# Optimization experiments

Measured on AMD Instinct MI355X. Metric: run time of the kernel, lower is better.

The kernel has to match this reference:

```python
import jax
import jax.numpy as jnp
import numpy as np
from jax import lax

B, NS, T, H, V = 4, 96, 8, 256, 32000
L = NS * T
N = NS + 1                    # num_nodes = num_statements + 1 (exit node)
NUM_LAYERS = NS // 16         # avg_statements_per_step = 16 -> 6 execution steps


def _lstm(c, h, x, Wx, Wh, b):
    """flax-style LSTM cell: gates in (i, f, g, o) order."""
    z = x @ Wx + h @ Wh + b
    gi, gf, gg, go = jnp.split(z, 4, axis=-1)
    c2 = jax.nn.sigmoid(gf) * c + jax.nn.sigmoid(gi) * jnp.tanh(gg)
    h2 = jax.nn.sigmoid(go) * jnp.tanh(c2)
    return c2, h2


def _forward(code_statements, code_length, embed, Wx_s, Wh_s, b_s, W_se, b_se,
             Wx_e, Wh_e, b_e, W_hk, b_hk, W_sd, b_sd, W_d1, b_d1, init_a, init_b):
    # ---- statement embedding: LSTM over the T tokens of each statement ----
    tok = embed[code_statements.astype(jnp.int32)]            # [B, L, H]
    tok = jnp.transpose(tok.reshape(B * NS, T, H), (1, 0, 2))  # [T, B*NS, H]
    c0 = jnp.zeros((B * NS, H), tok.dtype)

    def scan_fn(carry, x):
        c, hh = carry
        c, hh = _lstm(c, hh, x, Wx_s, Wh_s, b_s)
        return (c, hh), None

    (_, h_last), _ = lax.scan(scan_fn, (c0, c0), tok)
    stmt = h_last.reshape(B, NS, H)                           # [B, NS, H]

    # ---- skip encoder: pairwise segment-sum embedding for skipping i -> j ----
    node = jnp.concatenate([stmt, jnp.zeros((B, 1, H), stmt.dtype)], axis=1)  # [B,N,H]
    pref = jnp.concatenate(
        [jnp.zeros((B, 1, H), stmt.dtype), jnp.cumsum(node, axis=1)], axis=1)[:, :N]
    skip = (pref[:, None, :, :] - pref[:, :, None, :]) @ W_se + b_se  # [B,N,N,H]

    stmt_len = (code_length // T).astype(jnp.int32)           # exit node index per example

    # ---- execution loop with soft instruction pointer ----
    c = jnp.broadcast_to(init_a, (B, N, H))
    h = jnp.broadcast_to(init_b, (B, N, H))
    p = jnp.zeros((B, N)).at[:, 0].set(1.0)

    def step(c, h, p, skip_nnh, length, layer):
        # per-example: c,h [N,H]; p [N]; skip_nnh [N,N,H]; length scalar
        n = p.shape[0]
        ar = jnp.arange(n)
        if layer == 0:
            mask = jnp.zeros((n, n)).at[:, 1].set(1.0)
        elif layer == NUM_LAYERS - 1:
            mask = jnp.zeros((n, n)).at[:, length].set(1.0)   # force skip to exit
        else:
            mask = 1.0 - jnp.tri(n)                           # strictly forward skips
            mask = jnp.where(ar <= length, mask, 0.0)         # no skips past exit
            mask = mask.at[:, length].set(1.0)                # always allow exit

        # skip attention logits
        skip_keys = skip_nnh @ W_sd + b_sd                    # [N,N,H]
        h_key = h @ W_hk + b_hk                               # [N,H]
        act = jax.nn.relu(jnp.concatenate(
            [jnp.broadcast_to(h_key[:, None, :], (n, n, H)), skip_keys], axis=-1))
        skip_logits = jnp.squeeze(act @ W_d1, -1) + b_d1[0]   # [N,N]
        skip_logits = jnp.where(mask > 0, skip_logits, -jnp.inf)
        skip_p = jax.nn.softmax(skip_logits, axis=-1)

        # one LSTM skip-execution step for every (i, j) pair, vectorized
        z = skip_nnh @ Wx_e + (h @ Wh_e)[:, None, :] + b_e    # [N,N,4H]
        gi, gf, gg, go = jnp.split(z, 4, axis=-1)
        c_prop = jax.nn.sigmoid(gf) * c[:, None, :] + jax.nn.sigmoid(gi) * jnp.tanh(gg)
        h_prop = jax.nn.sigmoid(go) * jnp.tanh(c_prop)
        fwd_edge = (ar[None, :] > ar[:, None])[:, :, None]    # only j > i executes
        c_prop = jnp.where(fwd_edge, c_prop, c[:, None, :])
        h_prop = jnp.where(fwd_edge, h_prop, h[:, None, :])
        valid = (mask[:, :, None] > 0) & (p[:, None, None] > 0)
        c_prop = jnp.where(valid, c_prop, 0.0)
        h_prop = jnp.where(valid, h_prop, 0.0)

        # soft aggregation of proposals weighted by p(i) * skip_p(i -> j)
        w = skip_p * p[:, None]                               # [N,N]
        denom = (w.sum(axis=0) + 1e-7)[:, None]               # [N,1]
        c_new = jnp.einsum('ijh,ij->jh', c_prop, w) / denom
        h_new = jnp.einsum('ijh,ij->jh', h_prop, w) / denom
        p_new = p @ skip_p
        return c_new, h_new, p_new

    for layer in range(NUM_LAYERS):
        c, h, p = jax.vmap(step, in_axes=(0, 0, 0, 0, 0, None))(
            c, h, p, skip, stmt_len, layer)
    return h                                                  # [B, N, H]


def setup_inputs() -> dict:
    key = jax.random.key(0)
    ks = jax.random.split(key, 16)

    def dense(k, fi, fo):
        return jax.random.normal(k, (fi, fo)) * (1.0 / np.sqrt(fi))

    return {
        'code_statements': jax.random.randint(ks[0], (B, L), 0, V, dtype=jnp.int32),
        'code_length': jax.random.randint(ks[1], (B,), 64, L, dtype=jnp.int32),
        'embed': jax.random.normal(ks[2], (V, H)) * 0.02,
        'Wx_s': dense(ks[3], H, 4 * H), 'Wh_s': dense(ks[4], H, 4 * H),
        'b_s': jnp.zeros((4 * H,)),
        'W_se': dense(ks[5], H, H), 'b_se': jnp.zeros((H,)),
        'Wx_e': dense(ks[6], H, 4 * H), 'Wh_e': dense(ks[7], H, 4 * H),
        'b_e': jnp.zeros((4 * H,)),
        'W_hk': dense(ks[8], H, H), 'b_hk': jnp.zeros((H,)),
        'W_sd': dense(ks[9], H, H), 'b_sd': jnp.zeros((H,)),
        'W_d1': dense(ks[10], 2 * H, 1), 'b_d1': jnp.zeros((1,)),
        'init_a': jax.random.normal(ks[11], (H,)),
        'init_b': jax.random.normal(ks[12], (H,)),
    }


def reference(code_statements, code_length, embed, Wx_s, Wh_s, b_s, W_se, b_se,
              Wx_e, Wh_e, b_e, W_hk, b_hk, W_sd, b_sd, W_d1, b_d1, init_a, init_b):
    return _forward(code_statements, code_length, embed, Wx_s, Wh_s, b_s, W_se, b_se,
                    Wx_e, Wh_e, b_e, W_hk, b_hk, W_sd, b_sd, W_d1, b_d1, init_a, init_b)
```

## Files before the change

### kernel.cpp

```cpp
#include <hip/hip_runtime.h>
#include <cstddef>

#define B_   4
#define NS_  96
#define T_   8
#define H_   256
#define N_   97
#define NL_  6
#define R_   388

__device__ __forceinline__ float sigm(float x) {
    return __builtin_amdgcn_rcpf(1.0f + __builtin_amdgcn_exp2f(-1.44269504f * x));
}
__device__ __forceinline__ float tanh_f(float x) {
    return 1.0f - 2.0f * __builtin_amdgcn_rcpf(1.0f + __builtin_amdgcn_exp2f(2.88539008f * x));
}

__device__ __forceinline__ void fma16(float4 a, float4 w0, float4 w1, float4 w2,
                                      float4 w3, float* acc) {
    acc[0] = fmaf(a.x, w0.x, acc[0]); acc[1] = fmaf(a.x, w0.y, acc[1]);
    acc[2] = fmaf(a.x, w0.z, acc[2]); acc[3] = fmaf(a.x, w0.w, acc[3]);
    acc[0] = fmaf(a.y, w1.x, acc[0]); acc[1] = fmaf(a.y, w1.y, acc[1]);
    acc[2] = fmaf(a.y, w1.z, acc[2]); acc[3] = fmaf(a.y, w1.w, acc[3]);
    acc[0] = fmaf(a.z, w2.x, acc[0]); acc[1] = fmaf(a.z, w2.y, acc[1]);
    acc[2] = fmaf(a.z, w2.z, acc[2]); acc[3] = fmaf(a.z, w2.w, acc[3]);
    acc[0] = fmaf(a.w, w3.x, acc[0]); acc[1] = fmaf(a.w, w3.y, acc[1]);
    acc[2] = fmaf(a.w, w3.z, acc[2]); acc[3] = fmaf(a.w, w3.w, acc[3]);
}

__global__ __launch_bounds__(512) void prologue(
        const int* __restrict__ ids, const float* __restrict__ embed,
        const float* __restrict__ Wx_s, const float* __restrict__ b_s,
        const float* __restrict__ b_se, const float* __restrict__ Wx_e,
        const float* __restrict__ b_e, const float* __restrict__ W_sd,
        const float* __restrict__ b_sd, const float* __restrict__ Wh_e,
        const float* __restrict__ init_a, const float* __restrict__ init_b,
        float* __restrict__ xz, float* __restrict__ cz, float* __restrict__ ck,
        float* __restrict__ hw, float* __restrict__ c0, float* __restrict__ h0,
        float* __restrict__ p0) {
    int bid = blockIdx.x, t = threadIdx.x;
    if (bid < 384) {
        __shared__ float As[64][260];
        __shared__ int ridx[64];
        int r0 = (bid >> 3) * 64, n0 = (bid & 7) * 128;
        if (t < 64) ridx[t] = ids[r0 + t];
        __syncthreads();
#pragma unroll
        for (int m = 0; m < 8; m++) {
            int L = m * 512 + t;
            int r = L >> 6, c4 = (L & 63) * 4;
            *(float4*)&As[r][c4] = *(const float4*)(embed + (size_t)ridx[r] * 256 + c4);
        }
        __syncthreads();
        int rg = t >> 5, cg = t & 31;
        float acc[4][4] = {};
        const float* wp = Wx_s + n0 + 4 * cg;
#pragma unroll 4
        for (int kb = 0; kb < 64; kb++) {
            float4 w0 = *(const float4*)(wp + (size_t)(4 * kb + 0) * 1024);
            float4 w1 = *(const float4*)(wp + (size_t)(4 * kb + 1) * 1024);
            float4 w2 = *(const float4*)(wp + (size_t)(4 * kb + 2) * 1024);
            float4 w3 = *(const float4*)(wp + (size_t)(4 * kb + 3) * 1024);
#pragma unroll
            for (int i = 0; i < 4; i++) {
                float4 a = *(const float4*)&As[rg * 4 + i][4 * kb];
                fma16(a, w0, w1, w2, w3, acc[i]);
            }
        }
        int col = n0 + 4 * cg;
        float4 bv = *(const float4*)&b_s[col];
#pragma unroll
        for (int i = 0; i < 4; i++) {
            int r = r0 + rg * 4 + i;
            float4 o = make_float4(acc[i][0] + bv.x, acc[i][1] + bv.y,
                                   acc[i][2] + bv.z, acc[i][3] + bv.w);
            *(float4*)&xz[(size_t)r * 1024 + col] = o;
        }
    } else if (bid < 386) {
        int n = (bid - 384) * 512 + t;
        float acc = b_e[n];
        for (int k = 0; k < 256; k++) acc = fmaf(b_se[k], Wx_e[(size_t)k * 1024 + n], acc);
        cz[n] = acc;
    } else if (bid < 388) {
        int n = (bid - 386) * 512 + t;
        float acc = b_e[n];
        for (int k = 0; k < 256; k++) {
            acc = fmaf(b_se[k], Wx_e[(size_t)k * 1024 + n], acc);
            acc = fmaf(init_b[k], Wh_e[(size_t)k * 1024 + n], acc);
        }
        hw[n] = acc;
    } else if (bid == 388) {
        if (t < 256) {
            float acc = b_sd[t];
            for (int k = 0; k < 256; k++) acc = fmaf(b_se[k], W_sd[(size_t)k * 256 + t], acc);
            ck[t] = acc;
        }
    } else {
        int r0 = (bid - 389) * 8 + (t >> 8) * 4;
        int col = t & 255;
        float ia = init_a[col], ib = init_b[col];
#pragma unroll
        for (int rr = 0; rr < 4; rr++) {
            int row = r0 + rr;
            if (row < R_) {
                c0[(size_t)row * 256 + col] = ia;
                h0[(size_t)row * 256 + col] = ib;
                if (col == 0) p0[row] = ((row % N_) == 0) ? 1.0f : 0.0f;
            }
        }
    }
}

__global__ __launch_bounds__(256) void lstm_first(const float* __restrict__ xz,
        const float* __restrict__ Wh, float* __restrict__ hbuf, float* __restrict__ cbuf) {
    __shared__ float Wh_s[256][64];
    __shared__ float h_s[32][260];
    __shared__ float zs[32][68];
    int t = threadIdx.x;
    int ct = blockIdx.x, st = blockIdx.y;
    int et0 = ct * 16, s0 = st * 32;
#pragma unroll
    for (int m = 0; m < 16; m++) {
        int L = m * 256 + t;
        int k = L >> 4, f = L & 15;
        int gg = f >> 2, qq = f & 3;
        *(float4*)&Wh_s[k][f * 4] = *(const float4*)&Wh[(size_t)k * 1024 + gg * 256 + et0 + qq * 4];
    }
    for (int seq = 0; seq < 32; seq++) {
        const float* z0 = xz + ((size_t)(s0 + seq) * T_) * 1024;
        float gi = z0[t], gg = z0[512 + t], go = z0[768 + t];
        float c0v = sigm(gi) * tanh_f(gg);
        h_s[seq][t] = sigm(go) * tanh_f(c0v);
    }
    float creg[2];
    {
        int sqA = t >> 4, e = et0 + (t & 15);
#pragma unroll
        for (int u = 0; u < 2; u++) {
            const float* z0 = xz + ((size_t)(s0 + sqA + u * 16) * T_) * 1024;
            creg[u] = sigm(z0[e]) * tanh_f(z0[512 + e]);
        }
    }
    __syncthreads();
    {
        int sp = (t >> 4) & 15, cq = t & 15;
        int g = cq >> 2, q4 = cq & 3;
        int gcol = g * 256 + et0 + q4 * 4;
        float4 a0 = *(const float4*)(xz + ((size_t)(s0 + sp) * T_ + 1) * 1024 + gcol);
        float4 a1 = *(const float4*)(xz + ((size_t)(s0 + sp + 16) * T_ + 1) * 1024 + gcol);
#pragma unroll 4
        for (int k = 0; k < 256; k++) {
            float4 w4 = *(const float4*)&Wh_s[k][cq * 4];
            float hA = h_s[sp][k];
            float hB = h_s[sp + 16][k];
            a0.x = fmaf(hA, w4.x, a0.x); a0.y = fmaf(hA, w4.y, a0.y);
            a0.z = fmaf(hA, w4.z, a0.z); a0.w = fmaf(hA, w4.w, a0.w);
            a1.x = fmaf(hB, w4.x, a1.x); a1.y = fmaf(hB, w4.y, a1.y);
            a1.z = fmaf(hB, w4.z, a1.z); a1.w = fmaf(hB, w4.w, a1.w);
        }
        *(float4*)&zs[sp][cq * 4] = a0;
        *(float4*)&zs[sp + 16][cq * 4] = a1;
    }
    __syncthreads();
    {
        int sqA = t >> 4, e = t & 15;
#pragma unroll
        for (int u = 0; u < 2; u++) {
            int seq = sqA + u * 16;
            float gi = zs[seq][e], gf = zs[seq][16 + e], gg = zs[seq][32 + e], go = zs[seq][48 + e];
            float cn = sigm(gf) * creg[u] + sigm(gi) * tanh_f(gg);
            size_t gidx = (size_t)(s0 + seq) * H_ + et0 + e;
            cbuf[gidx] = cn;
            hbuf[gidx] = sigm(go) * tanh_f(cn);
        }
    }
}

__global__ __launch_bounds__(256) void lstm_step(int step, const float* __restrict__ xz,
        const float* __restrict__ Wh, float* __restrict__ hbuf, float* __restrict__ cbuf) {
    __shared__ float Wh_s[256][64];
    __shared__ float h_s[32][260];
    __shared__ float zs[32][68];
    int t = threadIdx.x;
    int ct = blockIdx.x, st = blockIdx.y;
    int et0 = ct * 16, s0 = st * 32;
    int sp = t >> 4, cq = t & 15;
    int g = cq >> 2, q4 = cq & 3;
    int gcol = g * 256 + et0 + q4 * 4;
    float4 a0 = *(const float4*)(xz + ((size_t)(s0 + sp) * T_ + step) * 1024 + gcol);
    float4 a1 = *(const float4*)(xz + ((size_t)(s0 + sp + 16) * T_ + step) * 1024 + gcol);
#pragma unroll
    for (int m = 0; m < 16; m++) {
        int L = m * 256 + t;
        int k = L >> 4, f = L & 15;
        int gg = f >> 2, qq = f & 3;
        *(float4*)&Wh_s[k][f * 4] = *(const float4*)&Wh[(size_t)k * 1024 + gg * 256 + et0 + qq * 4];
    }
#pragma unroll
    for (int m = 0; m < 8; m++) {
        int L = m * 256 + t;
        int seq = L >> 6, c4 = (L & 63) * 4;
        *(float4*)&h_s[seq][c4] = *(const float4*)&hbuf[(size_t)(s0 + seq) * H_ + c4];
    }
    __syncthreads();
#pragma unroll 4
    for (int k = 0; k < 256; k++) {
        float4 w4 = *(const float4*)&Wh_s[k][cq * 4];
        float h0 = h_s[sp][k];
        float h1 = h_s[sp + 16][k];
        a0.x = fmaf(h0, w4.x, a0.x); a0.y = fmaf(h0, w4.y, a0.y);
        a0.z = fmaf(h0, w4.z, a0.z); a0.w = fmaf(h0, w4.w, a0.w);
        a1.x = fmaf(h1, w4.x, a1.x); a1.y = fmaf(h1, w4.y, a1.y);
        a1.z = fmaf(h1, w4.z, a1.z); a1.w = fmaf(h1, w4.w, a1.w);
    }
    *(float4*)&zs[sp][cq * 4] = a0;
    *(float4*)&zs[sp + 16][cq * 4] = a1;
    __syncthreads();
    int seqA = t >> 4, e = t & 15;
#pragma unroll
    for (int u = 0; u < 2; u++) {
        int seq = seqA + u * 16;
        float gi = zs[seq][e], gf = zs[seq][16 + e], gg = zs[seq][32 + e], go = zs[seq][48 + e];
        size_t gidx = (size_t)(s0 + seq) * H_ + et0 + e;
        float cnew = sigm(gf) * cbuf[gidx] + sigm(gi) * tanh_f(gg);
        cbuf[gidx] = cnew;
        hbuf[gidx] = sigm(go) * tanh_f(cnew);
    }
}

template<int MT>
__global__ __launch_bounds__(256) void gemm_t(const float* __restrict__ A,
        const float* __restrict__ W, const float* __restrict__ bias,
        const float* __restrict__ subQ, const float* __restrict__ pgate,
        float* __restrict__ C, int R, int NC) {
    __shared__ float As[MT][260];
    __shared__ int anyflag;
    int t = threadIdx.x;
    int n0 = blockIdx.x * 128;
    int r0 = blockIdx.y * MT;
    if (pgate) {
        if (t == 0) anyflag = 0;
        __syncthreads();
        if (t < MT && r0 + t < R && pgate[r0 + t] != 0.0f) anyflag = 1;
        __syncthreads();
        if (!anyflag) return;
    }
#pragma unroll
    for (int m = 0; m < MT / 4; m++) {
        int L = m * 256 + t;
        int r = L >> 6, c4 = (L & 63) * 4;
        int rr = r0 + r;
        float4 v = make_float4(0.f, 0.f, 0.f, 0.f);
        if (rr < R) v = *(const float4*)(A + (size_t)rr * 256 + c4);
        *(float4*)&As[r][c4] = v;
    }
    __syncthreads();
    constexpr int RT = MT / 8;
    int rg = t >> 5, cg = t & 31;
    float acc[RT][4] = {};
    const float* wp = W + n0 + 4 * cg;
#pragma unroll 2
    for (int kb = 0; kb < 64; kb++) {
        float4 w0 = *(const float4*)(wp + (size_t)(4 * kb + 0) * NC);
        float4 w1 = *(const float4*)(wp + (size_t)(4 * kb + 1) * NC);
        float4 w2 = *(const float4*)(wp + (size_t)(4 * kb + 2) * NC);
        float4 w3 = *(const float4*)(wp + (size_t)(4 * kb + 3) * NC);
#pragma unroll
        for (int i = 0; i < RT; i++) {
            float4 a = *(const float4*)&As[rg * RT + i][4 * kb];
            fma16(a, w0, w1, w2, w3, acc[i]);
        }
    }
    int col = n0 + 4 * cg;
    float4 bv = make_float4(0.f, 0.f, 0.f, 0.f);
    if (bias) bv = *(const float4*)&bias[col];
#pragma unroll
    for (int i = 0; i < RT; i++) {
        int r = r0 + rg * RT + i;
        if (r < R) {
            float4 o = make_float4(acc[i][0] + bv.x, acc[i][1] + bv.y,
                                   acc[i][2] + bv.z, acc[i][3] + bv.w);
            if (subQ) {
                float4 s4 = *(const float4*)(subQ + (size_t)r * NC + col);
                o.x -= s4.x; o.y -= s4.y; o.z -= s4.z; o.w -= s4.w;
            }
            *(float4*)&C[(size_t)r * NC + col] = o;
        }
    }
}

__global__ __launch_bounds__(256) void qr_kernel(const float* __restrict__ S,
        const float* __restrict__ Wx_e, const float* __restrict__ W_sd,
        const float* __restrict__ hw, float* __restrict__ q, float* __restrict__ ve0,
        float* __restrict__ r_, float* __restrict__ rT) {
    __shared__ float As[16][260];
    int t = threadIdx.x;
    int bx = blockIdx.x;
    int r0 = blockIdx.y * 16;
#pragma unroll
    for (int m = 0; m < 4; m++) {
        int L = m * 256 + t;
        int r = L >> 6, c4 = (L & 63) * 4;
        int rr = r0 + r;
        float4 v = make_float4(0.f, 0.f, 0.f, 0.f);
        if (rr < R_) v = *(const float4*)(S + (size_t)rr * 256 + c4);
        *(float4*)&As[r][c4] = v;
    }
    __syncthreads();
    bool isq = bx < 8;
    const float* W = isq ? Wx_e : W_sd;
    int NC = isq ? 1024 : 256;
    int n0 = (isq ? bx : bx - 8) * 128;
    int rg = t >> 5, cg = t & 31;
    float acc[2][4] = {};
    const float* wp = W + n0 + 4 * cg;
#pragma unroll 2
    for (int kb = 0; kb < 64; kb++) {
        float4 w0 = *(const float4*)(wp + (size_t)(4 * kb + 0) * NC);
        float4 w1 = *(const float4*)(wp + (size_t)(4 * kb + 1) * NC);
        float4 w2 = *(const float4*)(wp + (size_t)(4 * kb + 2) * NC);
        float4 w3 = *(const float4*)(wp + (size_t)(4 * kb + 3) * NC);
#pragma unroll
        for (int i = 0; i < 2; i++) {
            float4 a = *(const float4*)&As[rg * 2 + i][4 * kb];
            fma16(a, w0, w1, w2, w3, acc[i]);
        }
    }
    int col = n0 + 4 * cg;
#pragma unroll
    for (int i = 0; i < 2; i++) {
        int r = r0 + rg * 2 + i;
        if (r < R_) {
            float4 o = make_float4(acc[i][0], acc[i][1], acc[i][2], acc[i][3]);
            if (isq) {
                *(float4*)&q[(size_t)r * 1024 + col] = o;
                float4 hwv = *(const float4*)&hw[col];
                float4 v0 = make_float4(hwv.x - o.x, hwv.y - o.y, hwv.z - o.z, hwv.w - o.w);
                *(float4*)&ve0[(size_t)r * 1024 + col] = v0;
            } else {
                *(float4*)&r_[(size_t)r * 256 + col] = o;
                int b = r / N_, n = r - b * N_;
                rT[((size_t)b * 256 + col + 0) * 128 + n] = o.x;
                rT[((size_t)b * 256 + col + 1) * 128 + n] = o.y;
                rT[((size_t)b * 256 + col + 2) * 128 + n] = o.z;
                rT[((size_t)b * 256 + col + 3) * 128 + n] = o.w;
            }
        }
    }
}

__global__ __launch_bounds__(1024) void cumsum_k(const float* __restrict__ stmt,
                                                 float* __restrict__ pref) {
    __shared__ float buf[96][256];
    int b = blockIdx.x, t = threadIdx.x;
#pragma unroll
    for (int m = 0; m < 6; m++) {
        int L = m * 1024 + t;
        int r = L >> 6, c4 = (L & 63) * 4;
        *(float4*)&buf[r][c4] = *(const float4*)(stmt + ((size_t)b * NS_ + r) * 256 + c4);
    }
    __syncthreads();
    if (t < 256) {
        float run = 0.0f;
        pref[((size_t)b * N_) * H_ + t] = 0.0f;
        for (int n = 1; n < N_; n++) {
            run += buf[n - 1][t];
            pref[((size_t)b * N_ + n) * H_ + t] = run;
        }
    }
}

__global__ void softmax_once(const float* __restrict__ r, const float* __restrict__ rT,
                             const float* __restrict__ ck, const float* __restrict__ Wd1,
                             const int* __restrict__ code_length,
                             float* __restrict__ spT_mid, float* __restrict__ spT0,
                             float* __restrict__ spT5) {
    __shared__ float ri[H_], ckl[H_], wd[H_];
    __shared__ float part[8][128];
    __shared__ float red[4];
    int t = threadIdx.x;
    int j = t & 127, half = t >> 7;
    int bi = blockIdx.x;
    int b = bi / N_, i = bi % N_;
    if (t < H_) {
        ri[t] = r[(size_t)bi * H_ + t];
        ckl[t] = ck[t];
        wd[t] = Wd1[256 + t];
    }
    __syncthreads();
    int len = code_length[b] / T_;
    bool valid = (j < N_) && ((j > i && j <= len) || (j == len));
    float acc = 0.0f;
    if (valid) {
        const float* rTb = rT + (size_t)b * H_ * 128 + j;
        int h0 = half * 32;
#pragma unroll 4
        for (int hh = 0; hh < 32; hh++) {
            int h = h0 + hh;
            float v = rTb[(size_t)h * 128] - ri[h] + ckl[h];
            acc = fmaf(fmaxf(v, 0.0f), wd[h], acc);
        }
    }
    part[half][j] = acc;
    __syncthreads();
    float logit = -3.0e38f;
    if (t < 128) {
        if (valid)
            logit = part[0][j] + part[1][j] + part[2][j] + part[3][j]
                  + part[4][j] + part[5][j] + part[6][j] + part[7][j];
        float m = logit;
#pragma unroll
        for (int off = 32; off; off >>= 1) m = fmaxf(m, __shfl_xor(m, off));
        if ((t & 63) == 0) red[t >> 6] = m;
    }
    __syncthreads();
    float e = 0.0f;
    if (t < 128) {
        float m = fmaxf(red[0], red[1]);
        e = valid ? __builtin_amdgcn_exp2f(1.44269504f * (logit - m)) : 0.0f;
        float s = e;
#pragma unroll
        for (int off = 32; off; off >>= 1) s += __shfl_xor(s, off);
        if ((t & 63) == 0) red[2 + (t >> 6)] = s;
    }
    __syncthreads();
    if (t < 128 && j < N_) {
        float s = red[2] + red[3];
        size_t o = ((size_t)b * N_ + j) * 128 + i;
        spT_mid[o] = e / s;
        spT0[o] = (j == 1) ? 1.0f : 0.0f;
        spT5[o] = (j == len) ? 1.0f : 0.0f;
    }
}

__global__ __launch_bounds__(512) void aggregate(const float* __restrict__ q,
        const float* __restrict__ ve, const float* __restrict__ spT,
        const float* __restrict__ p, const float* __restrict__ cc,
        const float* __restrict__ hc, float* __restrict__ cn,
        float* __restrict__ hn, float* __restrict__ pn) {
    __shared__ float qj[1024];
    __shared__ float wcol[128];
    __shared__ int vlist[128];
    __shared__ int cnts[2];
    __shared__ float wsums[2];
    __shared__ float parts[2][2][H_];
    int t = threadIdx.x;
    int bj = blockIdx.x;
    int b = bj / N_, j = bj - b * N_;
    bool pred = false;
    int rank = 0;
    if (t < 128) {
        float wv = (t < N_) ? spT[(size_t)bj * 128 + t] * p[b * N_ + t] : 0.f;
        wcol[t] = wv;
        float s = wv;
#pragma unroll
        for (int off = 32; off; off >>= 1) s += __shfl_xor(s, off);
        pred = (wv != 0.0f);
        unsigned long long mask = __ballot(pred);
        int lane = t & 63;
        rank = __popcll(mask & ((1ull << lane) - 1ull));
        if (lane == 0) { cnts[t >> 6] = (int)__popcll(mask); wsums[t >> 6] = s; }
    }
    __syncthreads();
    float wsum = wsums[0] + wsums[1];
    int nv = cnts[0] + cnts[1];
    if (t < 128 && pred) vlist[(t >= 64 ? cnts[0] : 0) + rank] = t;
    if (wsum == 0.0f) {
        if (t < 256) {
            cn[(size_t)bj * H_ + t] = 0.0f;
            hn[(size_t)bj * H_ + t] = 0.0f;
            if (t == 0) pn[bj] = 0.0f;
        }
        return;
    }
    qj[t] = q[(size_t)bj * 1024 + t];
    qj[512 + t] = q[(size_t)bj * 1024 + 512 + t];
    __syncthreads();
    int hh = t & 255, vs = t >> 8;
    float ac = 0.f, ah = 0.f;
    for (int v = vs; v < nv; v += 2) {
        int i = vlist[v];
        float wv = wcol[i];
        size_t rowi = (size_t)b * N_ + i;
        if (j > i) {
            const float* vei = ve + rowi * 1024;
            float gi = qj[hh] + vei[hh];
            float gf = qj[256 + hh] + vei[256 + hh];
            float gg = qj[512 + hh] + vei[512 + hh];
            float go = qj[768 + hh] + vei[768 + hh];
            float c2 = cc[rowi * H_ + hh];
            float cp = sigm(gf) * c2 + sigm(gi) * tanh_f(gg);
            float hp = sigm(go) * tanh_f(cp);
            ac = fmaf(wv, cp, ac);
            ah = fmaf(wv, hp, ah);
        } else {
            ac = fmaf(wv, cc[rowi * H_ + hh], ac);
            ah = fmaf(wv, hc[rowi * H_ + hh], ah);
        }
    }
    parts[vs][0][hh] = ac;
    parts[vs][1][hh] = ah;
    __syncthreads();
    if (t < 256) {
        float inv = __builtin_amdgcn_rcpf(wsum + 1e-7f);
        cn[(size_t)bj * H_ + t] = (parts[0][0][t] + parts[1][0][t]) * inv;
        hn[(size_t)bj * H_ + t] = (parts[0][1][t] + parts[1][1][t]) * inv;
        if (t == 0) pn[bj] = wsum;
    }
}


extern "C" void kernel_launch(void* const* d_in, const int* in_sizes, int n_in,
                              void* d_out, int out_size, void* d_ws, size_t ws_size,
                              hipStream_t stream) {
    const int*   code_statements = (const int*)d_in[0];
    const int*   code_length = (const int*)d_in[1];
    const float* embed = (const float*)d_in[2];
    const float* Wx_s = (const float*)d_in[3];
    const float* Wh_s = (const float*)d_in[4];
    const float* b_s  = (const float*)d_in[5];
    const float* W_se = (const float*)d_in[6];
    const float* b_se = (const float*)d_in[7];
    const float* Wx_e = (const float*)d_in[8];
    const float* Wh_e = (const float*)d_in[9];
    const float* b_e  = (const float*)d_in[10];
    const float* W_sd = (const float*)d_in[13];
    const float* b_sd = (const float*)d_in[14];
    const float* W_d1 = (const float*)d_in[15];
    const float* init_a = (const float*)d_in[17];
    const float* init_b = (const float*)d_in[18];
    float* out = (float*)d_out;

    float* wsf = (float*)d_ws;
    size_t off = 0;
    auto alloc = [&](size_t n) { float* p = wsf + off; off += n; return p; };
    float* cz = alloc(1024);
    float* ck = alloc(256);
    float* hw = alloc(1024);
    float* xz = alloc((size_t)3072 * 1024);
    float* stmt = alloc(384 * 256);
    float* cls = alloc(384 * 256);
    float* pref = alloc(R_ * 256);
    float* s_   = alloc(R_ * 256);
    float* q  = alloc(R_ * 1024);
    float* r_ = alloc(R_ * 256);
    float* rT = alloc(4 * 256 * 128);
    float* ve = alloc(R_ * 1024);
    float* spT_mid = alloc(R_ * 128);
    float* spT0    = alloc(R_ * 128);
    float* spT5    = alloc(R_ * 128);
    float* p0 = alloc(R_);
    float* p1 = alloc(R_);
    float* c0 = alloc(R_ * 256);
    float* c1 = alloc(R_ * 256);
    float* h0 = alloc(R_ * 256);
    float* h1 = alloc(R_ * 256);

    prologue<<<dim3(438), 512, 0, stream>>>(code_statements, embed, Wx_s, b_s,
                                            b_se, Wx_e, b_e, W_sd, b_sd, Wh_e,
                                            init_a, init_b, xz, cz, ck, hw, c0, h0, p0);
    lstm_first<<<dim3(16, 12), 256, 0, stream>>>(xz, Wh_s, stmt, cls);
    for (int step = 2; step < T_; step++)
        lstm_step<<<dim3(16, 12), 256, 0, stream>>>(step, xz, Wh_s, stmt, cls);
    cumsum_k<<<dim3(4), 1024, 0, stream>>>(stmt, pref);
    gemm_t<16><<<dim3(2, 25), 256, 0, stream>>>(pref, W_se, nullptr, nullptr, nullptr,
                                                s_, R_, 256);
    qr_kernel<<<dim3(10, 25), 256, 0, stream>>>(s_, Wx_e, W_sd, hw, q, ve, r_, rT);
    softmax_once<<<dim3(R_), 1024, 0, stream>>>(r_, rT, ck, W_d1, code_length,
                                                spT_mid, spT0, spT5);

    for (int layer = 0; layer < NL_; layer++) {
        bool odd = (layer & 1);
        float* pc = odd ? p1 : p0;
        float* pn = odd ? p0 : p1;
        float* cc = odd ? c1 : c0;
        float* cn = odd ? c0 : c1;
        float* hc = odd ? h1 : h0;
        float* hn = odd ? h0 : h1;
        if (layer == NL_ - 1) hn = out;
        const float* spT = (layer == 0) ? spT0 : (layer == NL_ - 1) ? spT5 : spT_mid;
        aggregate<<<dim3(R_), 512, 0, stream>>>(q, ve, spT, pc, cc, hc, cn, hn, pn);
        if (layer < NL_ - 1)
            gemm_t<16><<<dim3(8, 25), 256, 0, stream>>>(hn, Wh_e, cz, q, pn,
                                                        ve, R_, 1024);
    }
}
```

Measured before the change: 382.1 us.

## Fuse statement-LSTM timesteps into one persistent kernel and shrink GEMM row tiles

Replaces the per-timestep lstm_first/lstm_step launches with a single lstm_all kernel. Each block owns four sequences, keeps the cell state in registers and h in shared memory across all timesteps, and streams Wh from global/L2 instead of staging it in LDS. This removes six kernel launches and the global round trips of h and c between steps, but leaves only 96 blocks, each reading the full Wh matrix every step. It also halves the row tile of the gemm_t launches so more blocks are spawned, and adds a min-blocks hint to the prologue launch bounds.

```diff
diff --git a/kernel.cpp b/kernel.cpp
--- a/kernel.cpp
+++ b/kernel.cpp
@@ -28,7 +28,7 @@
     acc[2] = fmaf(a.w, w3.z, acc[2]); acc[3] = fmaf(a.w, w3.w, acc[3]);
 }
 
-__global__ __launch_bounds__(512) void prologue(
+__global__ __launch_bounds__(512, 4) void prologue(
         const int* __restrict__ ids, const float* __restrict__ embed,
         const float* __restrict__ Wx_s, const float* __restrict__ b_s,
         const float* __restrict__ b_se, const float* __restrict__ Wx_e,
@@ -111,121 +111,55 @@
     }
 }
 
-__global__ __launch_bounds__(256) void lstm_first(const float* __restrict__ xz,
-        const float* __restrict__ Wh, float* __restrict__ hbuf, float* __restrict__ cbuf) {
-    __shared__ float Wh_s[256][64];
-    __shared__ float h_s[32][260];
-    __shared__ float zs[32][68];
+__global__ __launch_bounds__(256) void lstm_all(const float* __restrict__ xz,
+        const float* __restrict__ Wh, float* __restrict__ hbuf) {
+    __shared__ float h_s[4][260];
+    __shared__ float zl[4][4][260];
     int t = threadIdx.x;
-    int ct = blockIdx.x, st = blockIdx.y;
-    int et0 = ct * 16, s0 = st * 32;
-#pragma unroll
-    for (int m = 0; m < 16; m++) {
-        int L = m * 256 + t;
-        int k = L >> 4, f = L & 15;
-        int gg = f >> 2, qq = f & 3;
-        *(float4*)&Wh_s[k][f * 4] = *(const float4*)&Wh[(size_t)k * 1024 + gg * 256 + et0 + qq * 4];
-    }
-    for (int seq = 0; seq < 32; seq++) {
-        const float* z0 = xz + ((size_t)(s0 + seq) * T_) * 1024;
+    int s0 = blockIdx.x * 4;
+    int g0 = t >> 6, e0 = (t & 63) * 4;
+    float c[4];
+#pragma unroll
+    for (int s = 0; s < 4; s++) {
+        const float* z0 = xz + ((size_t)(s0 + s) * T_) * 1024;
         float gi = z0[t], gg = z0[512 + t], go = z0[768 + t];
-        float c0v = sigm(gi) * tanh_f(gg);
-        h_s[seq][t] = sigm(go) * tanh_f(c0v);
-    }
-    float creg[2];
-    {
-        int sqA = t >> 4, e = et0 + (t & 15);
-#pragma unroll
-        for (int u = 0; u < 2; u++) {
-            const float* z0 = xz + ((size_t)(s0 + sqA + u * 16) * T_) * 1024;
-            creg[u] = sigm(z0[e]) * tanh_f(z0[512 + e]);
-        }
-    }
-    __syncthreads();
-    {
-        int sp = (t >> 4) & 15, cq = t & 15;
-        int g = cq >> 2, q4 = cq & 3;
-        int gcol = g * 256 + et0 + q4 * 4;
-        float4 a0 = *(const float4*)(xz + ((size_t)(s0 + sp) * T_ + 1) * 1024 + gcol);
-        float4 a1 = *(const float4*)(xz + ((size_t)(s0 + sp + 16) * T_ + 1) * 1024 + gcol);
+        c[s] = sigm(gi) * tanh_f(gg);
+        h_s[s][t] = sigm(go) * tanh_f(c[s]);
+    }
+    __syncthreads();
+    for (int step = 1; step < T_; step++) {
+        float4 z[4];
+#pragma unroll
+        for (int s = 0; s < 4; s++)
+            z[s] = *(const float4*)(xz + ((size_t)(s0 + s) * T_ + step) * 1024 + 4 * t);
+        const float* wp = Wh + 4 * t;
 #pragma unroll 4
-        for (int k = 0; k < 256; k++) {
-            float4 w4 = *(const float4*)&Wh_s[k][cq * 4];
-            float hA = h_s[sp][k];
-            float hB = h_s[sp + 16][k];
-            a0.x = fmaf(hA, w4.x, a0.x); a0.y = fmaf(hA, w4.y, a0.y);
-            a0.z = fmaf(hA, w4.z, a0.z); a0.w = fmaf(hA, w4.w, a0.w);
-            a1.x = fmaf(hB, w4.x, a1.x); a1.y = fmaf(hB, w4.y, a1.y);
-            a1.z = fmaf(hB, w4.z, a1.z); a1.w = fmaf(hB, w4.w, a1.w);
-        }
-        *(float4*)&zs[sp][cq * 4] = a0;
-        *(float4*)&zs[sp + 16][cq * 4] = a1;
-    }
-    __syncthreads();
-    {
-        int sqA = t >> 4, e = t & 15;
-#pragma unroll
-        for (int u = 0; u < 2; u++) {
-            int seq = sqA + u * 16;
-            float gi = zs[seq][e], gf = zs[seq][16 + e], gg = zs[seq][32 + e], go = zs[seq][48 + e];
-            float cn = sigm(gf) * creg[u] + sigm(gi) * tanh_f(gg);
-            size_t gidx = (size_t)(s0 + seq) * H_ + et0 + e;
-            cbuf[gidx] = cn;
-            hbuf[gidx] = sigm(go) * tanh_f(cn);
-        }
-    }
-}
-
-__global__ __launch_bounds__(256) void lstm_step(int step, const float* __restrict__ xz,
-        const float* __restrict__ Wh, float* __restrict__ hbuf, float* __restrict__ cbuf) {
-    __shared__ float Wh_s[256][64];
-    __shared__ float h_s[32][260];
-    __shared__ float zs[32][68];
-    int t = threadIdx.x;
-    int ct = blockIdx.x, st = blockIdx.y;
-    int et0 = ct * 16, s0 = st * 32;
-    int sp = t >> 4, cq = t & 15;
-    int g = cq >> 2, q4 = cq & 3;
-    int gcol = g * 256 + et0 + q4 * 4;
-    float4 a0 = *(const float4*)(xz + ((size_t)(s0 + sp) * T_ + step) * 1024 + gcol);
-    float4 a1 = *(const float4*)(xz + ((size_t)(s0 + sp + 16) * T_ + step) * 1024 + gcol);
-#pragma unroll
-    for (int m = 0; m < 16; m++) {
-        int L = m * 256 + t;
-        int k = L >> 4, f = L & 15;
-        int gg = f >> 2, qq = f & 3;
-        *(float4*)&Wh_s[k][f * 4] = *(const float4*)&Wh[(size_t)k * 1024 + gg * 256 + et0 + qq * 4];
-    }
-#pragma unroll
-    for (int m = 0; m < 8; m++) {
-        int L = m * 256 + t;
-        int seq = L >> 6, c4 = (L & 63) * 4;
-        *(float4*)&h_s[seq][c4] = *(const float4*)&hbuf[(size_t)(s0 + seq) * H_ + c4];
-    }
-    __syncthreads();
-#pragma unroll 4
-    for (int k = 0; k < 256; k++) {
-        float4 w4 = *(const float4*)&Wh_s[k][cq * 4];
-        float h0 = h_s[sp][k];
-        float h1 = h_s[sp + 16][k];
-        a0.x = fmaf(h0, w4.x, a0.x); a0.y = fmaf(h0, w4.y, a0.y);
-        a0.z = fmaf(h0, w4.z, a0.z); a0.w = fmaf(h0, w4.w, a0.w);
-        a1.x = fmaf(h1, w4.x, a1.x); a1.y = fmaf(h1, w4.y, a1.y);
-        a1.z = fmaf(h1, w4.z, a1.z); a1.w = fmaf(h1, w4.w, a1.w);
-    }
-    *(float4*)&zs[sp][cq * 4] = a0;
-    *(float4*)&zs[sp + 16][cq * 4] = a1;
-    __syncthreads();
-    int seqA = t >> 4, e = t & 15;
-#pragma unroll
-    for (int u = 0; u < 2; u++) {
-        int seq = seqA + u * 16;
-        float gi = zs[seq][e], gf = zs[seq][16 + e], gg = zs[seq][32 + e], go = zs[seq][48 + e];
-        size_t gidx = (size_t)(s0 + seq) * H_ + et0 + e;
-        float cnew = sigm(gf) * cbuf[gidx] + sigm(gi) * tanh_f(gg);
-        cbuf[gidx] = cnew;
-        hbuf[gidx] = sigm(go) * tanh_f(cnew);
-    }
+        for (int kb = 0; kb < 64; kb++) {
+            float4 w0 = *(const float4*)(wp + (size_t)(4 * kb + 0) * 1024);
+            float4 w1 = *(const float4*)(wp + (size_t)(4 * kb + 1) * 1024);
+            float4 w2 = *(const float4*)(wp + (size_t)(4 * kb + 2) * 1024);
+            float4 w3 = *(const float4*)(wp + (size_t)(4 * kb + 3) * 1024);
+#pragma unroll
+            for (int s = 0; s < 4; s++) {
+                float4 a = *(const float4*)&h_s[s][4 * kb];
+                fma16(a, w0, w1, w2, w3, (float*)&z[s]);
+            }
+        }
+#pragma unroll
+        for (int s = 0; s < 4; s++)
+            *(float4*)&zl[s][g0][e0] = z[s];
+        __syncthreads();
+#pragma unroll
+        for (int s = 0; s < 4; s++) {
+            float gi = zl[s][0][t], gf = zl[s][1][t], gg = zl[s][2][t], go = zl[s][3][t];
+            c[s] = sigm(gf) * c[s] + sigm(gi) * tanh_f(gg);
+            h_s[s][t] = sigm(go) * tanh_f(c[s]);
+        }
+        __syncthreads();
+    }
+#pragma unroll
+    for (int s = 0; s < 4; s++)
+        hbuf[(size_t)(s0 + s) * H_ + t] = h_s[s][t];
 }
 
 template<int MT>
@@ -539,7 +473,6 @@
     float* hw = alloc(1024);
     float* xz = alloc((size_t)3072 * 1024);
     float* stmt = alloc(384 * 256);
-    float* cls = alloc(384 * 256);
     float* pref = alloc(R_ * 256);
     float* s_   = alloc(R_ * 256);
     float* q  = alloc(R_ * 1024);
@@ -559,12 +492,10 @@
     prologue<<<dim3(438), 512, 0, stream>>>(code_statements, embed, Wx_s, b_s,
                                             b_se, Wx_e, b_e, W_sd, b_sd, Wh_e,
                                             init_a, init_b, xz, cz, ck, hw, c0, h0, p0);
-    lstm_first<<<dim3(16, 12), 256, 0, stream>>>(xz, Wh_s, stmt, cls);
-    for (int step = 2; step < T_; step++)
-        lstm_step<<<dim3(16, 12), 256, 0, stream>>>(step, xz, Wh_s, stmt, cls);
+    lstm_all<<<dim3(96), 256, 0, stream>>>(xz, Wh_s, stmt);
     cumsum_k<<<dim3(4), 1024, 0, stream>>>(stmt, pref);
-    gemm_t<16><<<dim3(2, 25), 256, 0, stream>>>(pref, W_se, nullptr, nullptr, nullptr,
-                                                s_, R_, 256);
+    gemm_t<8><<<dim3(2, 49), 256, 0, stream>>>(pref, W_se, nullptr, nullptr, nullptr,
+                                               s_, R_, 256);
     qr_kernel<<<dim3(10, 25), 256, 0, stream>>>(s_, Wx_e, W_sd, hw, q, ve, r_, rT);
     softmax_once<<<dim3(R_), 1024, 0, stream>>>(r_, rT, ck, W_d1, code_length,
                                                 spT_mid, spT0, spT5);
@@ -581,7 +512,7 @@
         const float* spT = (layer == 0) ? spT0 : (layer == NL_ - 1) ? spT5 : spT_mid;
         aggregate<<<dim3(R_), 512, 0, stream>>>(q, ve, spT, pc, cc, hc, cn, hn, pn);
         if (layer < NL_ - 1)
-            gemm_t<16><<<dim3(8, 25), 256, 0, stream>>>(hn, Wh_e, cz, q, pn,
-                                                        ve, R_, 1024);
-    }
-}
+            gemm_t<8><<<dim3(8, 49), 256, 0, stream>>>(hn, Wh_e, cz, q, pn,
+                                                       ve, R_, 1024);
+    }
+}
```

Result: slower. 455.8 us (+19.3%).
